# Kernel tuning notes

Measured on AMD Instinct MI355X. Metric: run time of the kernel, lower is better.

## Reference

```python
import jax, jax.numpy as jnp
import numpy as np

D_MODEL = 1024
NUM_HEADS = 16
HEAD_DIM = D_MODEL // NUM_HEADS
D_FF = 4 * D_MODEL


def _linear_params(key, d_in, d_out):
    kw, kb = jax.random.split(key)
    bound = 1.0 / np.sqrt(d_in)
    W = jax.random.uniform(kw, (d_in, d_out), minval=-bound, maxval=bound, dtype=jnp.float32)
    b = jax.random.uniform(kb, (d_out,), minval=-bound, maxval=bound, dtype=jnp.float32)
    return W, b


def setup_inputs() -> dict:
    key = jax.random.key(0)
    ks = jax.random.split(key, 6)
    x = jax.random.normal(ks[0], (4, 2048, D_MODEL), dtype=jnp.float32)
    qkv_w, qkv_b = _linear_params(ks[1], D_MODEL, 3 * D_MODEL)
    out_w, out_b = _linear_params(ks[2], D_MODEL, D_MODEL)
    ffn1_w, ffn1_b = _linear_params(ks[3], D_MODEL, D_FF)
    ffn2_w, ffn2_b = _linear_params(ks[4], D_FF, D_MODEL)
    ln1_g = jnp.ones((D_MODEL,), jnp.float32); ln1_b = jnp.zeros((D_MODEL,), jnp.float32)
    ln2_g = jnp.ones((D_MODEL,), jnp.float32); ln2_b = jnp.zeros((D_MODEL,), jnp.float32)
    return {
        "x": x,
        "qkv_w": qkv_w, "qkv_b": qkv_b,
        "out_w": out_w, "out_b": out_b,
        "ffn1_w": ffn1_w, "ffn1_b": ffn1_b,
        "ffn2_w": ffn2_w, "ffn2_b": ffn2_b,
        "ln1_g": ln1_g, "ln1_b": ln1_b,
        "ln2_g": ln2_g, "ln2_b": ln2_b,
    }


def _layer_norm(x, g, b, eps=1e-5):
    mu = jnp.mean(x, axis=-1, keepdims=True)
    var = jnp.mean(jnp.square(x - mu), axis=-1, keepdims=True)
    return (x - mu) * jax.lax.rsqrt(var + eps) * g + b


def reference(x, qkv_w, qkv_b, out_w, out_b, ffn1_w, ffn1_b, ffn2_w, ffn2_b,
              ln1_g, ln1_b, ln2_g, ln2_b):
    B, S, D = x.shape
    H, Hd = NUM_HEADS, HEAD_DIM
    normed = _layer_norm(x, ln1_g, ln1_b)
    qkv = normed @ qkv_w + qkv_b                      # [B,S,3D]
    qkv = qkv.reshape(B, S, 3, H, Hd)
    q = jnp.transpose(qkv[:, :, 0], (0, 2, 1, 3))     # [B,H,S,Hd]
    k = jnp.transpose(qkv[:, :, 1], (0, 2, 1, 3))
    v = jnp.transpose(qkv[:, :, 2], (0, 2, 1, 3))
    scores = jnp.einsum('bhqd,bhkd->bhqk', q, k) / np.sqrt(Hd).astype(np.float32)
    causal = jnp.tril(jnp.ones((S, S), dtype=bool))
    scores = jnp.where(causal[None, None], scores, -jnp.inf)
    attn = jax.nn.softmax(scores, axis=-1)
    attn_out = jnp.einsum('bhqk,bhkd->bhqd', attn, v)  # [B,H,S,Hd]
    attn_out = jnp.transpose(attn_out, (0, 2, 1, 3)).reshape(B, S, D)
    attn_out = attn_out @ out_w + out_b
    x = x + attn_out
    h = _layer_norm(x, ln2_g, ln2_b)
    h = jax.nn.gelu(h @ ffn1_w + ffn1_b, approximate=False)
    h = h @ ffn2_w + ffn2_b
    return x + h
```

## Files before the change

### kernel.cpp

```cpp
#include <hip/hip_runtime.h>
#include <hip/hip_bf16.h>
#include <math.h>

typedef __attribute__((ext_vector_type(8))) short short8;
typedef __attribute__((ext_vector_type(4))) float f32x4;

__device__ __forceinline__ float bf2f(unsigned short u) {
    union { unsigned int i; float f; } c; c.i = ((unsigned int)u) << 16; return c.f;
}
__device__ __forceinline__ unsigned short f2bf(float f) {
    union { float f; unsigned int i; } c; c.f = f;
    unsigned int i = c.i;
    unsigned int r = (i + 0x7FFFu + ((i >> 16) & 1u)) >> 16;
    return (unsigned short)r;
}
__device__ __forceinline__ float fexp2(float x) { return __builtin_amdgcn_exp2f(x); }

__device__ __forceinline__ void gload16(const unsigned short* g, unsigned short* l) {
    __builtin_amdgcn_global_load_lds(
        (const __attribute__((address_space(1))) unsigned int*)g,
        (__attribute__((address_space(3))) unsigned int*)l, 16, 0, 0);
}

__device__ __forceinline__ void load8(const unsigned short* p, float* v) {
    short8 s = *(const short8*)p;
#pragma unroll
    for (int i = 0; i < 8; i++) v[i] = bf2f((unsigned short)s[i]);
}
__device__ __forceinline__ void load8(const float* p, float* v) {
    f32x4 a = ((const f32x4*)p)[0], b = ((const f32x4*)p)[1];
    v[0] = a[0]; v[1] = a[1]; v[2] = a[2]; v[3] = a[3];
    v[4] = b[0]; v[5] = b[1]; v[6] = b[2]; v[7] = b[3];
}
__device__ __forceinline__ void store8(unsigned short* p, const float* v) {
    short8 s;
#pragma unroll
    for (int i = 0; i < 8; i++) s[i] = (short)f2bf(v[i]);
    *(short8*)p = s;
}
__device__ __forceinline__ void store8(float* p, const float* v) {
    f32x4 a, b;
    a[0] = v[0]; a[1] = v[1]; a[2] = v[2]; a[3] = v[3];
    b[0] = v[4]; b[1] = v[5]; b[2] = v[6]; b[3] = v[7];
    ((f32x4*)p)[0] = a; ((f32x4*)p)[1] = b;
}

__global__ __launch_bounds__(256) void ln_f32_kernel(
    const float* __restrict__ x, const float* __restrict__ g,
    const float* __restrict__ b, unsigned short* __restrict__ out) {
    const int row = blockIdx.x;
    const int t = threadIdx.x;
    const float* xr = x + (size_t)row * 1024;
    float4 raw = ((const float4*)xr)[t];
    float v0 = raw.x, v1 = raw.y, v2 = raw.z, v3 = raw.w;
    float s = v0 + v1 + v2 + v3;
    float ss = v0 * v0 + v1 * v1 + v2 * v2 + v3 * v3;
    for (int off = 32; off > 0; off >>= 1) {
        s += __shfl_down(s, off);
        ss += __shfl_down(ss, off);
    }
    __shared__ float red[8];
    __shared__ float stat[2];
    const int wave = t >> 6, lane = t & 63;
    if (lane == 0) { red[wave] = s; red[4 + wave] = ss; }
    __syncthreads();
    if (t == 0) {
        float st = red[0] + red[1] + red[2] + red[3];
        float sst = red[4] + red[5] + red[6] + red[7];
        float mu = st * (1.0f / 1024.0f);
        float var = sst * (1.0f / 1024.0f) - mu * mu;
        stat[0] = mu; stat[1] = rsqrtf(var + 1e-5f);
    }
    __syncthreads();
    const float mu = stat[0], rstd = stat[1];
    float4 gr = ((const float4*)g)[t];
    float4 br = ((const float4*)b)[t];
    ushort4 o;
    o.x = f2bf((v0 - mu) * rstd * gr.x + br.x);
    o.y = f2bf((v1 - mu) * rstd * gr.y + br.y);
    o.z = f2bf((v2 - mu) * rstd * gr.z + br.z);
    o.w = f2bf((v3 - mu) * rstd * gr.w + br.w);
    ((ushort4*)(out + (size_t)row * 1024))[t] = o;
}

__global__ __launch_bounds__(256) void ln_bf16_kernel(
    const unsigned short* __restrict__ x, const float* __restrict__ g,
    const float* __restrict__ b, unsigned short* __restrict__ out) {
    const int row = blockIdx.x;
    const int t = threadIdx.x;
    const unsigned short* xr = x + (size_t)row * 1024;
    ushort4 raw = ((const ushort4*)xr)[t];
    float v0 = bf2f(raw.x), v1 = bf2f(raw.y), v2 = bf2f(raw.z), v3 = bf2f(raw.w);
    float s = v0 + v1 + v2 + v3;
    float ss = v0 * v0 + v1 * v1 + v2 * v2 + v3 * v3;
    for (int off = 32; off > 0; off >>= 1) {
        s += __shfl_down(s, off);
        ss += __shfl_down(ss, off);
    }
    __shared__ float red[8];
    __shared__ float stat[2];
    const int wave = t >> 6, lane = t & 63;
    if (lane == 0) { red[wave] = s; red[4 + wave] = ss; }
    __syncthreads();
    if (t == 0) {
        float st = red[0] + red[1] + red[2] + red[3];
        float sst = red[4] + red[5] + red[6] + red[7];
        float mu = st * (1.0f / 1024.0f);
        float var = sst * (1.0f / 1024.0f) - mu * mu;
        stat[0] = mu; stat[1] = rsqrtf(var + 1e-5f);
    }
    __syncthreads();
    const float mu = stat[0], rstd = stat[1];
    float4 gr = ((const float4*)g)[t];
    float4 br = ((const float4*)b)[t];
    ushort4 o;
    o.x = f2bf((v0 - mu) * rstd * gr.x + br.x);
    o.y = f2bf((v1 - mu) * rstd * gr.y + br.y);
    o.z = f2bf((v2 - mu) * rstd * gr.z + br.z);
    o.w = f2bf((v3 - mu) * rstd * gr.w + br.w);
    ((ushort4*)(out + (size_t)row * 1024))[t] = o;
}

__global__ __launch_bounds__(256) void transpose_cast_kernel(
    const float* __restrict__ in, unsigned short* __restrict__ out, int R, int C) {
    __shared__ unsigned short tile[32][33];
    const int bx = blockIdx.x * 32, by = blockIdx.y * 32;
    const int tx = threadIdx.x & 31, ty = threadIdx.x >> 5;
    for (int i = 0; i < 32; i += 8)
        tile[ty + i][tx] = f2bf(in[(size_t)(by + ty + i) * C + bx + tx]);
    __syncthreads();
    for (int i = 0; i < 32; i += 8)
        out[(size_t)(bx + ty + i) * R + by + tx] = tile[tx][ty + i];
}

enum { EPI_QKV = 0, EPI_RES = 1, EPI_GELU = 2 };

template <int BN, int EPI, typename RT, typename OT>
__global__ __launch_bounds__(512, 2) void gemm256(
    const unsigned short* __restrict__ A, const unsigned short* __restrict__ Bt,
    const float* __restrict__ bias, const RT* __restrict__ res,
    OT* __restrict__ o0, unsigned short* __restrict__ o1,
    unsigned short* __restrict__ o2, int M, int N, int K) {
    constexpr int NFRAG = BN / 64;
    constexpr int NF2 = NFRAG / 2;
    constexpr int BQ = BN / 64;
    constexpr int ASZ = 16384;
    constexpr int BSZ = BN * 64;
    constexpr int BUFSH = ASZ + BSZ;
    constexpr int PE = BN + 8;
    __shared__ __align__(16) unsigned short SMEM[2 * BUFSH];
    const int t = threadIdx.x;
    const int wave = t >> 6, lane = t & 63;
    const int lr = lane & 15, lq = lane >> 4;
    const int wm = wave >> 2, wn = wave & 3;
    const int m0 = blockIdx.y * 256, n0 = blockIdx.x * BN;
    const int swz16 = (lr & 4) << 2;
    f32x4 acc[8][NFRAG] = {};
    short8 a[4][2], b[NF2][2];
    const int tswz = (t * 16) ^ (((t >> 5) & 1) << 5);
    const int srow = tswz >> 7;
    const int scol = (tswz & 127) >> 1;
    const unsigned short* agS = A + (size_t)(m0 + srow) * K + scol;
    const unsigned short* bgS = Bt + (size_t)(n0 + srow) * K + scol;
    const size_t q64K = (size_t)64 * K;

#define STAGE(ktv, dv) do {                                                   \
    unsigned short* dA_ = SMEM + (dv) * BUFSH;                                \
    unsigned short* dB_ = dA_ + ASZ;                                          \
    const int ko_ = (ktv) << 6;                                               \
    _Pragma("unroll") for (int qi = 0; qi < 4; ++qi)                          \
        gload16(agS + (size_t)qi * q64K + ko_, dA_ + qi * 4096 + t * 8);      \
    _Pragma("unroll") for (int qi = 0; qi < BQ; ++qi)                         \
        gload16(bgS + (size_t)qi * q64K + ko_, dB_ + qi * 4096 + t * 8);      \
} while (0)

#define READ_A(qm) do {                                                       \
    _Pragma("unroll") for (int mi = 0; mi < 4; ++mi) {                        \
        const int rA_ = wm * 128 + (qm) * 64 + mi * 16 + lr;                  \
        _Pragma("unroll") for (int ks = 0; ks < 2; ++ks)                      \
            a[mi][ks] = *(const short8*)(Ash + ((rA_ * 64 + ks * 32 + lq * 8) ^ swz16)); \
    } } while (0)

#define READ_B(qn) do {                                                       \
    _Pragma("unroll") for (int ni = 0; ni < NF2; ++ni) {                      \
        const int rB_ = wn * (BN / 4) + (qn) * (BN / 8) + ni * 16 + lr;       \
        _Pragma("unroll") for (int ks = 0; ks < 2; ++ks)                      \
            b[ni][ks] = *(const short8*)(Bsh + ((rB_ * 64 + ks * 32 + lq * 8) ^ swz16)); \
    } } while (0)

#define MFMAQ(qm, qn) do {                                                    \
    _Pragma("unroll") for (int mi = 0; mi < 4; ++mi)                          \
        _Pragma("unroll") for (int ni = 0; ni < NF2; ++ni) {                  \
            f32x4 c_ = acc[(qm) * 4 + mi][(qn) * NF2 + ni];                   \
            c_ = __builtin_amdgcn_mfma_f32_16x16x32_bf16(a[mi][0], b[ni][0], c_, 0, 0, 0); \
            c_ = __builtin_amdgcn_mfma_f32_16x16x32_bf16(a[mi][1], b[ni][1], c_, 0, 0, 0); \
            acc[(qm) * 4 + mi][(qn) * NF2 + ni] = c_;                         \
        } } while (0)

    STAGE(0, 0);
    const int nkt = K >> 6;
    for (int kt = 0; kt < nkt; ++kt) {
        const unsigned short* Ash = SMEM + (kt & 1) * BUFSH;
        const unsigned short* Bsh = Ash + ASZ;
        asm volatile("s_waitcnt vmcnt(0)" ::: "memory");
        __builtin_amdgcn_s_barrier();
        __builtin_amdgcn_sched_barrier(0);
        READ_A(0);
        READ_B(0);
        if (kt + 1 < nkt) { STAGE(kt + 1, (kt + 1) & 1); }
        __builtin_amdgcn_s_barrier();
        __builtin_amdgcn_s_setprio(1); MFMAQ(0, 0); __builtin_amdgcn_s_setprio(0);
        __builtin_amdgcn_s_barrier();
        READ_B(1);
        __builtin_amdgcn_s_barrier();
        __builtin_amdgcn_s_setprio(1); MFMAQ(0, 1); __builtin_amdgcn_s_setprio(0);
        __builtin_amdgcn_s_barrier();
        READ_A(1);
        __builtin_amdgcn_s_barrier();
        __builtin_amdgcn_s_setprio(1); MFMAQ(1, 1); __builtin_amdgcn_s_setprio(0);
        __builtin_amdgcn_s_barrier();
        READ_B(0);
        __builtin_amdgcn_s_barrier();
        __builtin_amdgcn_s_setprio(1); MFMAQ(1, 0); __builtin_amdgcn_s_setprio(0);
    }
#undef STAGE
#undef READ_A
#undef READ_B
#undef MFMAQ

    __syncthreads();
    const bool vreg = (EPI == EPI_QKV) && (n0 >= 2048);
    for (int h = 0; h < 2; ++h) {
        if (h) __syncthreads();
        if (wm == h) {
#pragma unroll
            for (int nj = 0; nj < NFRAG; ++nj) {
                const int col = wn * (BN / 4) + nj * 16 + lr;
                const float bv = bias[n0 + col];
#pragma unroll
                for (int mi = 0; mi < 8; ++mi) {
#pragma unroll
                    for (int r = 0; r < 4; ++r) {
                        const int lrow = mi * 16 + lq * 4 + r;
                        float val = acc[mi][nj][r] + bv;
                        if (EPI == EPI_GELU)
                            val = 0.5f * val * (1.0f + erff(val * 0.70710678118654752f));
                        if (vreg) SMEM[col * 136 + lrow] = f2bf(val);
                        else      SMEM[lrow * PE + col] = f2bf(val);
                    }
                }
            }
        }
        __syncthreads();
        if (EPI == EPI_RES || EPI == EPI_GELU) {
            const int rr = t >> 2, sg = (t & 3) * (BN / 4);
            const size_t base = (size_t)(m0 + h * 128 + rr) * N + n0 + sg;
            const unsigned short* src = SMEM + rr * PE + sg;
#pragma unroll
            for (int j = 0; j < BN / 32; ++j) {
                float v[8];
                load8(src + j * 8, v);
                if (EPI == EPI_RES) {
                    float rv[8];
                    load8(res + base + j * 8, rv);
#pragma unroll
                    for (int i = 0; i < 8; i++) v[i] += rv[i];
                }
                store8(o0 + base + j * 8, v);
            }
        } else if (!vreg) {
            const int rr = t >> 2, sg = (t & 3) * 64;
            const int col0 = n0 + sg;
            const int which = col0 >> 10;
            const int hn = (col0 & 1023) >> 6;
            const int grow = m0 + h * 128 + rr;
            const size_t bh = (size_t)((grow >> 11) * 16 + hn);
            unsigned short* dst = ((which == 0) ? (unsigned short*)o0 : o1) +
                                  (bh * 2048 + (size_t)(grow & 2047)) * 64;
            const unsigned short* src = SMEM + rr * PE + sg;
#pragma unroll
            for (int j = 0; j < 8; ++j)
                *(short8*)(dst + j * 8) = *(const short8*)(src + j * 8);
        } else {
            const int c = t >> 1, rh = (t & 1) * 64;
            const int rem = n0 + c - 2048;
            const int hn = rem >> 6, dd = rem & 63;
            const size_t bh = (size_t)((m0 >> 11) * 16 + hn);
            unsigned short* dst = o2 + (bh * 64 + dd) * 2048 +
                                  (size_t)((m0 + h * 128 + rh) & 2047);
            const unsigned short* src = SMEM + c * 136 + rh;
#pragma unroll
            for (int j = 0; j < 8; ++j)
                *(short8*)(dst + j * 8) = *(const short8*)(src + j * 8);
        }
    }
}

__global__ __launch_bounds__(256) void attn_kernel(
    const unsigned short* __restrict__ qb, const unsigned short* __restrict__ kb,
    const unsigned short* __restrict__ vtb, unsigned short* __restrict__ aout) {
    const int bx = blockIdx.x;
    const int bh = blockIdx.y;
    const int bidx = bh >> 4, h = bh & 15;
    const int t = threadIdx.x, wave = t >> 6, lane = t & 63;
    const int lr = lane & 15, lq = lane >> 4;
    __shared__ __align__(16) unsigned short Ks[64 * 68];
    __shared__ __align__(16) unsigned short Vs[64 * 68];
    __shared__ __align__(16) unsigned short Ps[4][32 * 68];
    const unsigned short* kbase = kb + (size_t)bh * 2048 * 64;
    const unsigned short* vbase = vtb + (size_t)bh * 64 * 2048;
    const int srow = t >> 3, scol = (t & 7) * 8;
    const float kQScale = 0.125f * 1.44269504088896f;

    for (int phase = 0; phase < 2; phase++) {
        const int qblk = phase ? (15 - bx) : bx;
        const unsigned short* qbase = qb + ((size_t)bh * 2048 + qblk * 128 + wave * 32) * 64;
        short8 qf[2][2];
#pragma unroll
        for (int f = 0; f < 2; f++)
#pragma unroll
            for (int c = 0; c < 2; c++) {
                short8 raw = *(const short8*)(qbase + (f * 16 + lr) * 64 + c * 32 + lq * 8);
                short8 sc;
#pragma unroll
                for (int j = 0; j < 8; j++)
                    sc[j] = (short)f2bf(bf2f((unsigned short)raw[j]) * kQScale);
                qf[f][c] = sc;
            }
        f32x4 acc[2][4] = {};
        float m_i[2][4], l_i[2][4];
#pragma unroll
        for (int f = 0; f < 2; f++)
#pragma unroll
            for (int r = 0; r < 4; r++) { m_i[f][r] = -1e30f; l_i[f][r] = 0.0f; }
        const int wave_q0 = qblk * 128 + wave * 32;
        const int nkt = 2 * (qblk + 1);
        short8 kr0 = *(const short8*)(kbase + t * 8);
        short8 kr1 = *(const short8*)(kbase + 2048 + t * 8);
        short8 vr0 = *(const short8*)(vbase + (size_t)srow * 2048 + scol);
        short8 vr1 = *(const short8*)(vbase + (size_t)(32 + srow) * 2048 + scol);
        for (int kt = 0; kt < nkt; kt++) {
            __syncthreads();
            *(short8*)(Ks + srow * 68 + scol) = kr0;
            *(short8*)(Ks + (32 + srow) * 68 + scol) = kr1;
            *(short8*)(Vs + srow * 68 + scol) = vr0;
            *(short8*)(Vs + (32 + srow) * 68 + scol) = vr1;
            __syncthreads();
            if (kt + 1 < nkt) {
                const unsigned short* kg = kbase + (kt + 1) * 4096;
                kr0 = *(const short8*)(kg + t * 8);
                kr1 = *(const short8*)(kg + 2048 + t * 8);
                vr0 = *(const short8*)(vbase + (size_t)srow * 2048 + (kt + 1) * 64 + scol);
                vr1 = *(const short8*)(vbase + (size_t)(32 + srow) * 2048 + (kt + 1) * 64 + scol);
            }
            if (kt * 64 <= wave_q0 + 31) {
                f32x4 sa[2][4];
#pragma unroll
                for (int ni = 0; ni < 4; ni++) {
                    short8 kf0 = *(const short8*)(Ks + (ni * 16 + lr) * 68 + lq * 8);
                    short8 kf1 = *(const short8*)(Ks + (ni * 16 + lr) * 68 + 32 + lq * 8);
#pragma unroll
                    for (int f = 0; f < 2; f++) {
                        f32x4 z = {};
                        z = __builtin_amdgcn_mfma_f32_16x16x32_bf16(qf[f][0], kf0, z, 0, 0, 0);
                        sa[f][ni] = __builtin_amdgcn_mfma_f32_16x16x32_bf16(qf[f][1], kf1, z, 0, 0, 0);
                    }
                }
                const bool needmask = (kt * 64 + 63 > wave_q0);
                if (needmask) {
#pragma unroll
                    for (int f = 0; f < 2; f++) {
                        const int qrow0 = wave_q0 + f * 16 + lq * 4;
#pragma unroll
                        for (int ni = 0; ni < 4; ni++) {
                            const int kcol = kt * 64 + ni * 16 + lr;
#pragma unroll
                            for (int r = 0; r < 4; r++)
                                if (kcol > qrow0 + r) sa[f][ni][r] = -1e30f;
                        }
                    }
                }
#pragma unroll
                for (int f = 0; f < 2; f++) {
                    float mcur[4], alpha[4], rsum[4];
#pragma unroll
                    for (int r = 0; r < 4; r++)
                        mcur[r] = fmaxf(fmaxf(sa[f][0][r], sa[f][1][r]), fmaxf(sa[f][2][r], sa[f][3][r]));
#pragma unroll
                    for (int r = 0; r < 4; r++) {
#pragma unroll
                        for (int off = 1; off < 16; off <<= 1) mcur[r] = fmaxf(mcur[r], __shfl_xor(mcur[r], off));
                        const float mn = fmaxf(m_i[f][r], mcur[r]);
                        alpha[r] = fexp2(m_i[f][r] - mn);
                        m_i[f][r] = mn;
                        rsum[r] = 0.0f;
                    }
#pragma unroll
                    for (int ni = 0; ni < 4; ni++)
#pragma unroll
                        for (int r = 0; r < 4; r++) {
                            const float p = fexp2(sa[f][ni][r] - m_i[f][r]);
                            Ps[wave][(f * 16 + lq * 4 + r) * 68 + ni * 16 + lr] = f2bf(p);
                            rsum[r] += p;
                        }
#pragma unroll
                    for (int r = 0; r < 4; r++) {
#pragma unroll
                        for (int off = 1; off < 16; off <<= 1) rsum[r] += __shfl_xor(rsum[r], off);
                        l_i[f][r] = l_i[f][r] * alpha[r] + rsum[r];
#pragma unroll
                        for (int ni = 0; ni < 4; ni++) acc[f][ni][r] *= alpha[r];
                    }
                }
                short8 pf[2][2];
#pragma unroll
                for (int f = 0; f < 2; f++)
#pragma unroll
                    for (int c = 0; c < 2; c++)
                        pf[f][c] = *(const short8*)(&Ps[wave][(f * 16 + lr) * 68 + c * 32 + lq * 8]);
#pragma unroll
                for (int ni = 0; ni < 4; ni++) {
                    short8 vf0 = *(const short8*)(Vs + (ni * 16 + lr) * 68 + lq * 8);
                    short8 vf1 = *(const short8*)(Vs + (ni * 16 + lr) * 68 + 32 + lq * 8);
#pragma unroll
                    for (int f = 0; f < 2; f++) {
                        acc[f][ni] = __builtin_amdgcn_mfma_f32_16x16x32_bf16(pf[f][0], vf0, acc[f][ni], 0, 0, 0);
                        acc[f][ni] = __builtin_amdgcn_mfma_f32_16x16x32_bf16(pf[f][1], vf1, acc[f][ni], 0, 0, 0);
                    }
                }
            }
        }
#pragma unroll
        for (int f = 0; f < 2; f++)
#pragma unroll
            for (int r = 0; r < 4; r++) {
                const float rinv = 1.0f / l_i[f][r];
                const int q = qblk * 128 + wave * 32 + f * 16 + lq * 4 + r;
                const size_t token = (size_t)bidx * 2048 + q;
#pragma unroll
                for (int ni = 0; ni < 4; ni++)
                    aout[token * 1024 + h * 64 + ni * 16 + lr] = f2bf(acc[f][ni][r] * rinv);
            }
    }
}

extern "C" void kernel_launch(void* const* d_in, const int* in_sizes, int n_in,
                              void* d_out, int out_size, void* d_ws, size_t ws_size,
                              hipStream_t stream) {
    const float* x      = (const float*)d_in[0];
    const float* qkv_w  = (const float*)d_in[1];
    const float* qkv_b  = (const float*)d_in[2];
    const float* out_w  = (const float*)d_in[3];
    const float* out_b  = (const float*)d_in[4];
    const float* ffn1_w = (const float*)d_in[5];
    const float* ffn1_b = (const float*)d_in[6];
    const float* ffn2_w = (const float*)d_in[7];
    const float* ffn2_b = (const float*)d_in[8];
    const float* ln1_g  = (const float*)d_in[9];
    const float* ln1_b  = (const float*)d_in[10];
    const float* ln2_g  = (const float*)d_in[11];
    const float* ln2_b  = (const float*)d_in[12];
    float* out = (float*)d_out;
    char* W = (char*)d_ws;

    unsigned short* normed = (unsigned short*)(W);
    unsigned short* x1     = (unsigned short*)(W + 16777216);
    unsigned short* qbuf   = (unsigned short*)(W + 33554432);
    unsigned short* kbuf   = (unsigned short*)(W + 50331648);
    unsigned short* vbuf   = (unsigned short*)(W + 67108864);
    unsigned short* attnb  = (unsigned short*)(W + 83886080);
    unsigned short* hff    = (unsigned short*)(W + 33554432);
    unsigned short* qkv_wt = (unsigned short*)(W + 100663296);
    unsigned short* out_wt = (unsigned short*)(W + 106954752);
    unsigned short* f1_wt  = (unsigned short*)(W + 109051904);
    unsigned short* f2_wt  = (unsigned short*)(W + 117440512);

    transpose_cast_kernel<<<dim3(3072 / 32, 1024 / 32), 256, 0, stream>>>(qkv_w, qkv_wt, 1024, 3072);
    transpose_cast_kernel<<<dim3(1024 / 32, 1024 / 32), 256, 0, stream>>>(out_w, out_wt, 1024, 1024);
    transpose_cast_kernel<<<dim3(4096 / 32, 1024 / 32), 256, 0, stream>>>(ffn1_w, f1_wt, 1024, 4096);
    transpose_cast_kernel<<<dim3(1024 / 32, 4096 / 32), 256, 0, stream>>>(ffn2_w, f2_wt, 4096, 1024);

    ln_f32_kernel<<<dim3(8192), 256, 0, stream>>>(x, ln1_g, ln1_b, normed);
    gemm256<256, EPI_QKV, float, unsigned short><<<dim3(3072 / 256, 8192 / 256), 512, 0, stream>>>(
        normed, qkv_wt, qkv_b, nullptr, qbuf, kbuf, vbuf, 8192, 3072, 1024);
    attn_kernel<<<dim3(8, 64), 256, 0, stream>>>(qbuf, kbuf, vbuf, attnb);
    gemm256<128, EPI_RES, float, unsigned short><<<dim3(1024 / 128, 8192 / 256), 512, 0, stream>>>(
        attnb, out_wt, out_b, x, x1, nullptr, nullptr, 8192, 1024, 1024);
    ln_bf16_kernel<<<dim3(8192), 256, 0, stream>>>(x1, ln2_g, ln2_b, normed);
    gemm256<256, EPI_GELU, float, unsigned short><<<dim3(4096 / 256, 8192 / 256), 512, 0, stream>>>(
        normed, f1_wt, ffn1_b, nullptr, hff, nullptr, nullptr, 8192, 4096, 1024);
    gemm256<128, EPI_RES, unsigned short, float><<<dim3(1024 / 128, 8192 / 256), 512, 0, stream>>>(
        hff, f2_wt, ffn2_b, x1, out, nullptr, nullptr, 8192, 1024, 4096);
}
```

Measured before the change: 651.2 us.

## Rework GEMM LDS swizzle, double-buffer B fragments, and narrow QKV tile

Replaces the old LDS XOR swizzle with a full 8-way row-based XOR of 16-byte chunks, meant to remove bank conflicts on fragment reads. B fragments now live in two register sets, so the fourth quadrant reuses the first B slice instead of reading it again from LDS, and the next-tile prefetch is issued before the first LDS reads. The QKV GEMM switches to a 128-wide N tile, with the epilogue generalized to BN, giving twice as many blocks. This costs more VGPRs for the extra B buffer and adds per-block overhead from the smaller QKV tile.

```diff
diff --git a/kernel.cpp b/kernel.cpp
--- a/kernel.cpp
+++ b/kernel.cpp
@@ -154,12 +154,11 @@
     const int lr = lane & 15, lq = lane >> 4;
     const int wm = wave >> 2, wn = wave & 3;
     const int m0 = blockIdx.y * 256, n0 = blockIdx.x * BN;
-    const int swz16 = (lr & 4) << 2;
+    const int xr3 = lr & 7;
     f32x4 acc[8][NFRAG] = {};
-    short8 a[4][2], b[NF2][2];
-    const int tswz = (t * 16) ^ (((t >> 5) & 1) << 5);
-    const int srow = tswz >> 7;
-    const int scol = (tswz & 127) >> 1;
+    short8 a[4][2], b0[NF2][2], b1[NF2][2];
+    const int srow = t >> 3;
+    const int scol = (((t & 7) ^ ((t >> 3) & 7)) << 3);
     const unsigned short* agS = A + (size_t)(m0 + srow) * K + scol;
     const unsigned short* bgS = Bt + (size_t)(n0 + srow) * K + scol;
     const size_t q64K = (size_t)64 * K;
@@ -178,22 +177,22 @@
     _Pragma("unroll") for (int mi = 0; mi < 4; ++mi) {                        \
         const int rA_ = wm * 128 + (qm) * 64 + mi * 16 + lr;                  \
         _Pragma("unroll") for (int ks = 0; ks < 2; ++ks)                      \
-            a[mi][ks] = *(const short8*)(Ash + ((rA_ * 64 + ks * 32 + lq * 8) ^ swz16)); \
+            a[mi][ks] = *(const short8*)(Ash + rA_ * 64 + (((ks * 4 + lq) ^ xr3) << 3)); \
     } } while (0)
 
-#define READ_B(qn) do {                                                       \
+#define READ_B(qn, barr) do {                                                 \
     _Pragma("unroll") for (int ni = 0; ni < NF2; ++ni) {                      \
         const int rB_ = wn * (BN / 4) + (qn) * (BN / 8) + ni * 16 + lr;       \
         _Pragma("unroll") for (int ks = 0; ks < 2; ++ks)                      \
-            b[ni][ks] = *(const short8*)(Bsh + ((rB_ * 64 + ks * 32 + lq * 8) ^ swz16)); \
+            barr[ni][ks] = *(const short8*)(Bsh + rB_ * 64 + (((ks * 4 + lq) ^ xr3) << 3)); \
     } } while (0)
 
-#define MFMAQ(qm, qn) do {                                                    \
+#define MFMAQ(qm, qn, barr) do {                                              \
     _Pragma("unroll") for (int mi = 0; mi < 4; ++mi)                          \
         _Pragma("unroll") for (int ni = 0; ni < NF2; ++ni) {                  \
             f32x4 c_ = acc[(qm) * 4 + mi][(qn) * NF2 + ni];                   \
-            c_ = __builtin_amdgcn_mfma_f32_16x16x32_bf16(a[mi][0], b[ni][0], c_, 0, 0, 0); \
-            c_ = __builtin_amdgcn_mfma_f32_16x16x32_bf16(a[mi][1], b[ni][1], c_, 0, 0, 0); \
+            c_ = __builtin_amdgcn_mfma_f32_16x16x32_bf16(a[mi][0], barr[ni][0], c_, 0, 0, 0); \
+            c_ = __builtin_amdgcn_mfma_f32_16x16x32_bf16(a[mi][1], barr[ni][1], c_, 0, 0, 0); \
             acc[(qm) * 4 + mi][(qn) * NF2 + ni] = c_;                         \
         } } while (0)
 
@@ -205,23 +204,21 @@
         asm volatile("s_waitcnt vmcnt(0)" ::: "memory");
         __builtin_amdgcn_s_barrier();
         __builtin_amdgcn_sched_barrier(0);
+        if (kt + 1 < nkt) { STAGE(kt + 1, (kt + 1) & 1); }
         READ_A(0);
-        READ_B(0);
-        if (kt + 1 < nkt) { STAGE(kt + 1, (kt + 1) & 1); }
-        __builtin_amdgcn_s_barrier();
-        __builtin_amdgcn_s_setprio(1); MFMAQ(0, 0); __builtin_amdgcn_s_setprio(0);
-        __builtin_amdgcn_s_barrier();
-        READ_B(1);
-        __builtin_amdgcn_s_barrier();
-        __builtin_amdgcn_s_setprio(1); MFMAQ(0, 1); __builtin_amdgcn_s_setprio(0);
+        READ_B(0, b0);
+        __builtin_amdgcn_s_barrier();
+        __builtin_amdgcn_s_setprio(1); MFMAQ(0, 0, b0); __builtin_amdgcn_s_setprio(0);
+        __builtin_amdgcn_s_barrier();
+        READ_B(1, b1);
+        __builtin_amdgcn_s_barrier();
+        __builtin_amdgcn_s_setprio(1); MFMAQ(0, 1, b1); __builtin_amdgcn_s_setprio(0);
         __builtin_amdgcn_s_barrier();
         READ_A(1);
         __builtin_amdgcn_s_barrier();
-        __builtin_amdgcn_s_setprio(1); MFMAQ(1, 1); __builtin_amdgcn_s_setprio(0);
-        __builtin_amdgcn_s_barrier();
-        READ_B(0);
-        __builtin_amdgcn_s_barrier();
-        __builtin_amdgcn_s_setprio(1); MFMAQ(1, 0); __builtin_amdgcn_s_setprio(0);
+        __builtin_amdgcn_s_setprio(1); MFMAQ(1, 1, b1); __builtin_amdgcn_s_setprio(0);
+        __builtin_amdgcn_s_barrier();
+        __builtin_amdgcn_s_setprio(1); MFMAQ(1, 0, b0); __builtin_amdgcn_s_setprio(0);
     }
 #undef STAGE
 #undef READ_A
@@ -269,20 +266,24 @@
                 store8(o0 + base + j * 8, v);
             }
         } else if (!vreg) {
-            const int rr = t >> 2, sg = (t & 3) * 64;
+            const int rr = t >> 2, sg = (t & 3) * (BN / 4);
             const int col0 = n0 + sg;
             const int which = col0 >> 10;
             const int hn = (col0 & 1023) >> 6;
+            const int dcol = col0 & 63;
             const int grow = m0 + h * 128 + rr;
             const size_t bh = (size_t)((grow >> 11) * 16 + hn);
             unsigned short* dst = ((which == 0) ? (unsigned short*)o0 : o1) +
-                                  (bh * 2048 + (size_t)(grow & 2047)) * 64;
+                                  (bh * 2048 + (size_t)(grow & 2047)) * 64 + dcol;
             const unsigned short* src = SMEM + rr * PE + sg;
 #pragma unroll
-            for (int j = 0; j < 8; ++j)
+            for (int j = 0; j < BN / 32; ++j)
                 *(short8*)(dst + j * 8) = *(const short8*)(src + j * 8);
         } else {
-            const int c = t >> 1, rh = (t & 1) * 64;
+            constexpr int TPC = 512 / BN;
+            constexpr int LTPC = (TPC == 2) ? 1 : 2;
+            constexpr int RSPAN = 128 / TPC;
+            const int c = t >> LTPC, rh = (t & (TPC - 1)) * RSPAN;
             const int rem = n0 + c - 2048;
             const int hn = rem >> 6, dd = rem & 63;
             const size_t bh = (size_t)((m0 >> 11) * 16 + hn);
@@ -290,7 +291,7 @@
                                   (size_t)((m0 + h * 128 + rh) & 2047);
             const unsigned short* src = SMEM + c * 136 + rh;
 #pragma unroll
-            for (int j = 0; j < 8; ++j)
+            for (int j = 0; j < RSPAN / 8; ++j)
                 *(short8*)(dst + j * 8) = *(const short8*)(src + j * 8);
         }
     }
@@ -481,7 +482,7 @@
     transpose_cast_kernel<<<dim3(1024 / 32, 4096 / 32), 256, 0, stream>>>(ffn2_w, f2_wt, 4096, 1024);
 
     ln_f32_kernel<<<dim3(8192), 256, 0, stream>>>(x, ln1_g, ln1_b, normed);
-    gemm256<256, EPI_QKV, float, unsigned short><<<dim3(3072 / 256, 8192 / 256), 512, 0, stream>>>(
+    gemm256<128, EPI_QKV, float, unsigned short><<<dim3(3072 / 128, 8192 / 256), 512, 0, stream>>>(
         normed, qkv_wt, qkv_b, nullptr, qbuf, kbuf, vbuf, 8192, 3072, 1024);
     attn_kernel<<<dim3(8, 64), 256, 0, stream>>>(qbuf, kbuf, vbuf, attnb);
     gemm256<128, EPI_RES, float, unsigned short><<<dim3(1024 / 128, 8192 / 256), 512, 0, stream>>>(
```

Result: faster. 613.7 us (-5.8%).
